# Performance work log

Measured on AMD Instinct MI355X. Metric: run time of the kernel, lower is better.

The kernel has to match this reference:

```python
import jax, jax.numpy as jnp
import numpy as np

N, T, H, L, E, F, CN, CG = 20000, 2, 128, 4, 320000, 514, 3, 2
EPS = 1e-7  # GENConv message epsilon


def _ln(x, g, b):
    mu = jnp.mean(x, axis=-1, keepdims=True)
    var = jnp.mean((x - mu) ** 2, axis=-1, keepdims=True)
    return (x - mu) / jnp.sqrt(var + 1e-5) * g + b


def _genconv(x, src, dst, e, W1, b1, g1, be1, W2, b2, t, n):
    # message: relu(x_j + edge_attr) + eps
    msg = jax.nn.relu(x[src] + e) + EPS  # [E,H]
    # softmax aggregation with learnable temperature t, grouped by dst
    logits = msg * t
    m = jax.ops.segment_max(logits, dst, num_segments=n)
    m = jnp.where(jnp.isfinite(m), m, 0.0)  # guard empty segments
    ex = jnp.exp(logits - m[dst])
    denom = jax.ops.segment_sum(ex, dst, num_segments=n)
    alpha = ex / (denom[dst] + 1e-16)
    agg = jax.ops.segment_sum(msg * alpha, dst, num_segments=n)  # [N,H]
    out = agg + x  # residual with root node (x_r)
    # MLP: Lin(H,2H) -> LayerNorm -> ReLU -> Lin(2H,H)
    h1 = jax.nn.relu(_ln(out @ W1 + b1, g1, be1))
    return h1 @ W2 + b2


def _attn(x, Wq, Wk, Wv, gamma):
    # x: [N, T, H]; channel (transform-axis) self-attention, gamma-gated residual
    q = jnp.einsum('tc,nch->nth', Wq, x)
    k = jnp.einsum('tc,nch->nth', Wk, x)
    v = jnp.einsum('tc,nch->nth', Wv, x)
    a = jax.nn.softmax(jnp.einsum('nth,nsh->nts', q, k), axis=-1)
    o = jnp.einsum('nts,nsh->nth', a, v)
    return gamma * o + x


def setup_inputs() -> dict:
    key = jax.random.key(0)
    ks = iter(jax.random.split(key, 48))

    def nrm(sh, s=0.02):
        return jax.random.normal(next(ks), sh, dtype=jnp.float32) * s

    inp = {}
    inp['node_feature'] = jax.random.normal(next(ks), (N, F), dtype=jnp.float32)
    inp['edge_index'] = jax.random.randint(next(ks), (T, 2, E), 0, N, dtype=jnp.int32)
    inp['edge_attr'] = jax.random.normal(next(ks), (T, E, 2), dtype=jnp.float32)
    # encoders
    inp['Wne'] = nrm((F, H)); inp['bne'] = jnp.zeros((H,), jnp.float32)
    inp['Wee'] = nrm((2, H)); inp['bee'] = jnp.zeros((H,), jnp.float32)
    # per-layer GENConv MLP params (stacked over L)
    inp['W1'] = nrm((L, H, 2 * H)); inp['b1'] = jnp.zeros((L, 2 * H), jnp.float32)
    inp['g1'] = jnp.ones((L, 2 * H), jnp.float32); inp['be1'] = jnp.zeros((L, 2 * H), jnp.float32)
    inp['W2'] = nrm((L, 2 * H, H)); inp['b2'] = jnp.zeros((L, H), jnp.float32)
    # DeepGCNLayer LayerNorms
    inp['dg'] = jnp.ones((L, H), jnp.float32); inp['db'] = jnp.zeros((L, H), jnp.float32)
    # learnable temperatures
    inp['t'] = jnp.ones((L,), jnp.float32)
    # node attention + head
    inp['Wq_n'] = nrm((T, T), 0.2); inp['Wk_n'] = nrm((T, T), 0.2); inp['Wv_n'] = nrm((T, T), 0.2)
    inp['gamma_n'] = jnp.float32(0.5)
    inp['Wn1'] = nrm((T * H, T * H)); inp['bn1'] = jnp.zeros((T * H,), jnp.float32)
    inp['Wn2'] = nrm((T * H, CN)); inp['bn2'] = jnp.zeros((CN,), jnp.float32)
    # graph attention + head
    inp['Wq_g'] = nrm((T, T), 0.2); inp['Wk_g'] = nrm((T, T), 0.2); inp['Wv_g'] = nrm((T, T), 0.2)
    inp['gamma_g'] = jnp.float32(0.5)
    inp['Wg1'] = nrm((T * H, T * H)); inp['bg1'] = jnp.zeros((T * H,), jnp.float32)
    inp['Wg2'] = nrm((T * H, CG)); inp['bg2'] = jnp.zeros((CG,), jnp.float32)
    return inp


def reference(node_feature, edge_index, edge_attr, Wne, bne, Wee, bee,
              W1, b1, g1, be1, W2, b2, dg, db, t,
              Wq_n, Wk_n, Wv_n, gamma_n, Wn1, bn1, Wn2, bn2,
              Wq_g, Wk_g, Wv_g, gamma_g, Wg1, bg1, Wg2, bg2):
    embs = []
    for ti in range(T):
        x = node_feature @ Wne + bne           # node_encoder
        e = edge_attr[ti] @ Wee + bee          # edge_encoder
        src, dst = edge_index[ti, 0], edge_index[ti, 1]
        # layers[0].conv applied directly
        x = _genconv(x, src, dst, e, W1[0], b1[0], g1[0], be1[0], W2[0], b2[0], t[0], N)
        # res+ DeepGCN blocks
        for l in range(1, L):
            h = jax.nn.relu(_ln(x, dg[l], db[l]))  # dropout p=0.1 is identity in eval
            x = x + _genconv(h, src, dst, e, W1[l], b1[l], g1[l], be1[l], W2[l], b2[l], t[l], N)
        x = jax.nn.relu(_ln(x, dg[0], db[0]))
        embs.append(x)
    emb = jnp.stack(embs, axis=1)  # [N, T, H]

    a = _attn(emb, Wq_n, Wk_n, Wv_n, gamma_n).reshape(N, T * H)
    node = jax.nn.relu(a @ Wn1 + bn1) @ Wn2 + bn2
    node = jax.nn.log_softmax(node, axis=-1)

    g = _attn(emb, Wq_g, Wk_g, Wv_g, gamma_g).reshape(N, T * H)
    gp = jnp.mean(g, axis=0, keepdims=True)  # global_mean_pool (single graph)
    gp = jax.nn.relu(gp @ Wg1 + bg1) @ Wg2 + bg2
    gp = jax.nn.log_softmax(gp, axis=-1)
    return (node, gp)
```

## Files before the change

kernel.cpp:

```cpp
#include <hip/hip_runtime.h>

#define NN 20000
#define TT 2
#define HH 128
#define LL 4
#define EE 320000
#define FF 514
#define CN 3
#define CG 2
#define EPS_MSG 1e-7f
#define MP 20096

typedef __bf16 bf16x8 __attribute__((ext_vector_type(8)));
typedef __bf16 bf16x4 __attribute__((ext_vector_type(4)));
typedef __bf16 bf16x2 __attribute__((ext_vector_type(2)));
typedef float f32x4 __attribute__((ext_vector_type(4)));

struct __align__(8) Edge { int src; __bf16 ea0, ea1; };

__device__ inline float wave_sum(float v) {
#pragma unroll
  for (int off = 32; off; off >>= 1) v += __shfl_xor(v, off);
  return v;
}
__device__ inline float red16(float v) {
  v += __shfl_xor(v, 1); v += __shfl_xor(v, 2);
  v += __shfl_xor(v, 4); v += __shfl_xor(v, 8);
  return v;
}

__device__ __forceinline__ float fexp2(float x) {
#if __has_builtin(__builtin_amdgcn_exp2f)
  return __builtin_amdgcn_exp2f(x);
#else
  return exp2f(x);
#endif
}

__device__ __forceinline__ void gload_lds16(const void* g, void* l) {
  __builtin_amdgcn_global_load_lds(
      (const __attribute__((address_space(1))) unsigned int*)g,
      (__attribute__((address_space(3))) unsigned int*)l, 16, 0, 0);
}

#define ENCB (MP / 64)
#define SCB 2500
#define CHUNK 5000
__global__ __launch_bounds__(256) void enc_scatter_kernel(
    const __bf16* __restrict__ A, const __bf16* __restrict__ BT,
    const float* __restrict__ bias, __bf16* __restrict__ C,
    const int* __restrict__ edge_index, const float* __restrict__ edge_attr,
    int* __restrict__ cursor, Edge* __restrict__ edges) {
  __shared__ __bf16 As[2][64][32];
  __shared__ __bf16 Bs[2][128][32];
  const int tid = threadIdx.x;
  if (blockIdx.x >= ENCB) {
    int chunk = blockIdx.x & 7;
    int i = ((blockIdx.x - ENCB) >> 3) * 256 + tid;
    if (i >= 2 * EE) return;
    int ti = (i >= EE) ? 1 : 0;
    int e = i - ti * EE;
    const int* srcp = edge_index + (size_t)ti * 2 * EE;
    int d = srcp[EE + e];
    int gnode = ti * NN + d;
    if (gnode / CHUNK != chunk) return;
    int s = srcp[e];
    float2 ea = ((const float2*)edge_attr)[(size_t)ti * EE + e];
    int pos = atomicAdd(&cursor[gnode], 1);
    Edge ed;
    ed.src = s + ti * MP;
    ed.ea0 = (__bf16)ea.x; ed.ea1 = (__bf16)ea.y;
    __builtin_memcpy(&edges[pos], &ed, sizeof(Edge));
    return;
  }
  const int K = 576;
  const int lane = tid & 63, w = tid >> 6;
  const int bm = blockIdx.x * 64;
  const int wr = (w >> 1) * 32, wc = (w & 1) * 64;
  const int fr = lane & 15, fq = lane >> 4;
  const int rowA = tid >> 2, chA = (tid & 3) * 8;
  const __bf16* Ab = A + (size_t)(bm + rowA) * K + chA;
  const __bf16* Bb = BT + (size_t)rowA * K + chA;
  const __bf16* Bb2 = Bb + (size_t)64 * K;
  f32x4 acc[2][4] = {};
#define STAGE(buf, k0)                                  \
  do {                                                  \
    gload_lds16(Ab + (k0), &As[buf][rowA][chA]);        \
    gload_lds16(Bb + (k0), &Bs[buf][rowA][chA]);        \
    gload_lds16(Bb2 + (k0), &Bs[buf][rowA + 64][chA]);  \
  } while (0)
  STAGE(0, 0);
  __syncthreads();
  int cur = 0;
  for (int k0 = 0; k0 < K; k0 += 32) {
    if (k0 + 32 < K) STAGE(cur ^ 1, k0 + 32);
    bf16x8 af[2], bq[4];
#pragma unroll
    for (int m = 0; m < 2; ++m)
      af[m] = *(const bf16x8*)&As[cur][wr + m * 16 + fr][fq * 8];
#pragma unroll
    for (int n = 0; n < 4; ++n)
      bq[n] = *(const bf16x8*)&Bs[cur][wc + n * 16 + fr][fq * 8];
#pragma unroll
    for (int m = 0; m < 2; ++m)
#pragma unroll
      for (int n = 0; n < 4; ++n)
        acc[m][n] =
            __builtin_amdgcn_mfma_f32_16x16x32_bf16(af[m], bq[n], acc[m][n], 0, 0, 0);
    __syncthreads();
    cur ^= 1;
  }
#undef STAGE
#pragma unroll
  for (int m = 0; m < 2; ++m) {
#pragma unroll
    for (int n = 0; n < 4; ++n) {
#pragma unroll
      for (int j = 0; j < 4; ++j) {
        int gm = bm + wr + m * 16 + fq * 4 + j;
        int gn = wc + n * 16 + fr;
        if (gm < NN) {
          __bf16 c = (__bf16)(acc[m][n][j] + bias[gn]);
          C[(size_t)gm * 128 + gn] = c;
          C[(size_t)(gm + MP) * 128 + gn] = c;
        }
      }
    }
  }
}

template <int EPI>
__global__ __launch_bounds__(256) void gemm256(
    const __bf16* __restrict__ A, const __bf16* __restrict__ BT,
    const float* __restrict__ bias, const float* __restrict__ g,
    const float* __restrict__ be, const float* __restrict__ W2h,
    const float* __restrict__ b2h, void* __restrict__ outp, int M, int K) {
  __shared__ __bf16 As[2][64][32];
  __shared__ __bf16 Bs[2][256][32];
  const int tid = threadIdx.x;
  const int lane = tid & 63, w = tid >> 6;
  const int bm = blockIdx.x * 64;
  const int wr = w * 16;
  const int fr = lane & 15, fq = lane >> 4;
  const int rowA = tid >> 2, chA = (tid & 3) * 8;
  const __bf16* Ab = A + (size_t)(bm + rowA) * K + chA;
  const __bf16* Bb = BT + (size_t)rowA * K + chA;
  f32x4 acc[16] = {};

#define STG(buf, k0)                                                \
  do {                                                              \
    gload_lds16(Ab + (k0), &As[buf][rowA][chA]);                    \
    _Pragma("unroll") for (int r = 0; r < 4; ++r)                   \
        gload_lds16(Bb + (size_t)(r * 64) * K + (k0),               \
                    &Bs[buf][rowA + r * 64][chA]);                  \
  } while (0)

  STG(0, 0);
  __syncthreads();
  int cur = 0;
  for (int k0 = 0; k0 < K; k0 += 32) {
    if (k0 + 32 < K) STG(cur ^ 1, k0 + 32);
    bf16x8 af = *(const bf16x8*)&As[cur][wr + fr][fq * 8];
#pragma unroll
    for (int n = 0; n < 16; ++n) {
      bf16x8 bq = *(const bf16x8*)&Bs[cur][n * 16 + fr][fq * 8];
      acc[n] = __builtin_amdgcn_mfma_f32_16x16x32_bf16(af, bq, acc[n], 0, 0, 0);
    }
    __syncthreads();
    cur ^= 1;
  }
#undef STG

  float cb[16];
#pragma unroll
  for (int n = 0; n < 16; ++n) cb[n] = bias[n * 16 + fr];

  if constexpr (EPI == 0) {
    float gv[16], bev[16];
#pragma unroll
    for (int n = 0; n < 16; ++n) {
      gv[n] = g[n * 16 + fr];
      bev[n] = be[n * 16 + fr];
    }
    __bf16* outb = (__bf16*)outp;
#pragma unroll
    for (int j = 0; j < 4; ++j) {
      float cj[16], s = 0.f, s2 = 0.f;
#pragma unroll
      for (int n = 0; n < 16; ++n) {
        float c = acc[n][j] + cb[n];
        cj[n] = c; s += c; s2 += c * c;
      }
      s = red16(s); s2 = red16(s2);
      float mu = s * (1.f / 256);
      float var = fmaxf(s2 * (1.f / 256) - mu * mu, 0.f);
      float rr = rsqrtf(var + 1e-5f);
      int gm = bm + wr + fq * 4 + j;
      __bf16* op = outb + (size_t)gm * 256;
#pragma unroll
      for (int n = 0; n < 16; ++n) {
        float y = (cj[n] - mu) * rr * gv[n] + bev[n];
        op[n * 16 + fr] = (__bf16)fmaxf(y, 0.f);
      }
    }
  } else {
    float w0[16], w1[16], w2[16];
#pragma unroll
    for (int n = 0; n < 16; ++n) {
      int col = n * 16 + fr;
      w0[n] = W2h[col * 3 + 0];
      w1[n] = W2h[col * 3 + 1];
      w2[n] = W2h[col * 3 + 2];
    }
    float* outf = (float*)outp;
#pragma unroll
    for (int j = 0; j < 4; ++j) {
      float p0 = 0.f, p1 = 0.f, p2 = 0.f;
#pragma unroll
      for (int n = 0; n < 16; ++n) {
        float h = fmaxf(acc[n][j] + cb[n], 0.f);
        p0 += h * w0[n]; p1 += h * w1[n]; p2 += h * w2[n];
      }
      p0 = red16(p0); p1 = red16(p1); p2 = red16(p2);
      int gm = bm + wr + fq * 4 + j;
      if (fr == 0 && gm < M) {
        float l0 = p0 + b2h[0], l1 = p1 + b2h[1], l2 = p2 + b2h[2];
        float m = fmaxf(l0, fmaxf(l1, l2));
        float lse = m + logf(__expf(l0 - m) + __expf(l1 - m) + __expf(l2 - m));
        outf[(size_t)gm * 3 + 0] = l0 - lse;
        outf[(size_t)gm * 3 + 1] = l1 - lse;
        outf[(size_t)gm * 3 + 2] = l2 - lse;
      }
    }
  }
}

template <int MODE>
__global__ __launch_bounds__(256) void gemm_lin2(
    const __bf16* __restrict__ A, const __bf16* __restrict__ BT,
    const float* __restrict__ bias, float* __restrict__ xres,
    const float* __restrict__ g, const float* __restrict__ be,
    void* __restrict__ lnout) {
  __shared__ __bf16 As[2][64][32];
  __shared__ __bf16 Bs[2][128][32];
  __shared__ float redS[64][2], redS2[64][2];
  const int tid = threadIdx.x;
  const int lane = tid & 63, w = tid >> 6;
  const int bm = blockIdx.x * 64;
  const int wr = (w >> 1) * 32, wc = (w & 1) * 64;
  const int fr = lane & 15, fq = lane >> 4;
  const int rowA = tid >> 2, chA = (tid & 3) * 8;
  const __bf16* Ab = A + (size_t)(bm + rowA) * 256 + chA;
  const __bf16* Bb = BT + (size_t)rowA * 256 + chA;
  const __bf16* Bb2 = Bb + (size_t)64 * 256;
  f32x4 acc[2][4] = {};

#define STAGE(buf, k0)                                  \
  do {                                                  \
    gload_lds16(Ab + (k0), &As[buf][rowA][chA]);        \
    gload_lds16(Bb + (k0), &Bs[buf][rowA][chA]);        \
    gload_lds16(Bb2 + (k0), &Bs[buf][rowA + 64][chA]);  \
  } while (0)

  STAGE(0, 0);
  __syncthreads();
  int cur = 0;
  for (int k0 = 0; k0 < 256; k0 += 32) {
    if (k0 + 32 < 256) STAGE(cur ^ 1, k0 + 32);
    bf16x8 af[2], bq[4];
#pragma unroll
    for (int m = 0; m < 2; ++m)
      af[m] = *(const bf16x8*)&As[cur][wr + m * 16 + fr][fq * 8];
#pragma unroll
    for (int n = 0; n < 4; ++n)
      bq[n] = *(const bf16x8*)&Bs[cur][wc + n * 16 + fr][fq * 8];
#pragma unroll
    for (int m = 0; m < 2; ++m)
#pragma unroll
      for (int n = 0; n < 4; ++n)
        acc[m][n] =
            __builtin_amdgcn_mfma_f32_16x16x32_bf16(af[m], bq[n], acc[m][n], 0, 0, 0);
    __syncthreads();
    cur ^= 1;
  }
#undef STAGE

  float cv[2][4][4];
#pragma unroll
  for (int m = 0; m < 2; ++m) {
    int r0 = wr + m * 16 + fq * 4;
#pragma unroll
    for (int j = 0; j < 4; ++j) {
      int gm = bm + r0 + j;
      float s = 0.f, s2 = 0.f;
#pragma unroll
      for (int n = 0; n < 4; ++n) {
        float c = acc[m][n][j] + bias[wc + n * 16 + fr];
        if (MODE != 0) c += xres[(size_t)gm * 128 + wc + n * 16 + fr];
        cv[m][n][j] = c;
        s += c; s2 += c * c;
      }
      s = red16(s); s2 = red16(s2);
      if (fr == 0) {
        redS[r0 + j][w & 1] = s;
        redS2[r0 + j][w & 1] = s2;
      }
    }
  }
  __syncthreads();
#pragma unroll
  for (int m = 0; m < 2; ++m) {
    int r0 = wr + m * 16 + fq * 4;
#pragma unroll
    for (int j = 0; j < 4; ++j) {
      int r = r0 + j;
      int gm = bm + r;
      float S = redS[r][0] + redS[r][1];
      float S2 = redS2[r][0] + redS2[r][1];
      float mu = S * (1.f / 128);
      float var = fmaxf(S2 * (1.f / 128) - mu * mu, 0.f);
      float rr = rsqrtf(var + 1e-5f);
      if constexpr (MODE < 2) {
        float* xp = xres + (size_t)gm * 128;
        __bf16* hp = (__bf16*)lnout + (size_t)gm * 128;
#pragma unroll
        for (int n = 0; n < 4; ++n) {
          int col = wc + n * 16 + fr;
          float c = cv[m][n][j];
          xp[col] = c;
          float y = (c - mu) * rr * g[col] + be[col];
          hp[col] = (__bf16)fmaxf(y, 0.f);
        }
      } else {
        int half = gm >= MP;
        int node = gm - half * MP;
        if (node < NN) {
          float* ep = (float*)lnout + (size_t)node * 256 + half * 128;
#pragma unroll
          for (int n = 0; n < 4; ++n) {
            int col = wc + n * 16 + fr;
            float y = (cv[m][n][j] - mu) * rr * g[col] + be[col];
            ep[col] = fmaxf(y, 0.f);
          }
        }
      }
    }
  }
}

struct WtDesc { const float* src; __bf16* dst; int K, N, Kpad; };
struct WtDescs { WtDesc d[10]; };
#define NF2B 20079
#define PADB 2422
#define WTB 2880
#define CNTB 2500

__global__ void prep_kernel(const float* __restrict__ nf_src,
                            __bf16* __restrict__ nf_dst, WtDescs descs,
                            const int* __restrict__ edge_index,
                            int* __restrict__ deg, float* __restrict__ gp_sum) {
  int b = blockIdx.x, tid = threadIdx.x;
  if (b < NF2B) {
    int i = b * 256 + tid;
    if (i >= NN * FF / 2) return;
    int row = i / 257;
    int col = (i - row * 257) * 2;
    float2 v = ((const float2*)nf_src)[i];
    bf16x2 o; o[0] = (__bf16)v.x; o[1] = (__bf16)v.y;
    *(bf16x2*)(nf_dst + (size_t)row * 576 + col) = o;
  } else if (b < NF2B + PADB) {
    int i = (b - NF2B) * 256 + tid;
    if (i >= NN * 31) return;
    int row = i / 31, j = i - row * 31;
    bf16x2 z; z[0] = (__bf16)0.f; z[1] = (__bf16)0.f;
    *(bf16x2*)(nf_dst + (size_t)row * 576 + 514 + 2 * j) = z;
  } else if (b < NF2B + PADB + WTB) {
    int wb = b - NF2B - PADB;
    WtDesc de = descs.d[wb / 288];
    int idx = (wb % 288) * 256 + tid;
    if (idx >= de.N * de.Kpad) return;
    int n = idx / de.Kpad, k = idx - n * de.Kpad;
    float v = (k < de.K) ? de.src[(size_t)k * de.N + n] : 0.f;
    de.dst[idx] = (__bf16)v;
  } else if (b < NF2B + PADB + WTB + CNTB) {
    int i = (b - NF2B - PADB - WTB) * 256 + tid;
    if (i >= 2 * EE) return;
    int ti = (i >= EE) ? 1 : 0;
    int e = i - ti * EE;
    int d = edge_index[(size_t)ti * 2 * EE + EE + e];
    atomicAdd(&deg[ti * NN + d], 1);
  } else {
    gp_sum[tid] = 0.f;
  }
}

__global__ __launch_bounds__(1024) void scan2_kernel(
    const int* __restrict__ deg_all, int* __restrict__ rowptr,
    int* __restrict__ cursor) {
  const int ti = blockIdx.x;
  const int* deg = deg_all + ti * NN;
  __shared__ int sums[1024];
  int tid = threadIdx.x;
  int chunk = (NN + 1023) / 1024;
  int begin = tid * chunk, end = min(begin + chunk, NN);
  int s = 0;
  for (int i = begin; i < end; ++i) s += deg[i];
  sums[tid] = s;
  __syncthreads();
  for (int off = 1; off < 1024; off <<= 1) {
    int v = (tid >= off) ? sums[tid - off] : 0;
    __syncthreads();
    sums[tid] += v;
    __syncthreads();
  }
  int running = ti * EE + sums[tid] - s;
  for (int i = begin; i < end; ++i) {
    rowptr[ti * NN + i] = running;
    cursor[ti * NN + i] = running;
    running += deg[i];
  }
  if (tid == 0 && ti == 1) rowptr[2 * NN] = 2 * EE;
}

__global__ __launch_bounds__(256) void agg_kernel(
    const __bf16* __restrict__ xin, const int* __restrict__ rowptr,
    const Edge* __restrict__ edges, const float* __restrict__ Wee,
    const float* __restrict__ bee, const float* __restrict__ tptr, int layer,
    __bf16* __restrict__ out) {
  int wave = threadIdx.x >> 6, lane = threadIdx.x & 63;
  int b = blockIdx.x;
  int x8 = b & 7;
  int q = x8 >> 1;
  int par = x8 & 1;
  int ti = q >> 1, chh = q & 1;
  int group = (b >> 3) * 2 + par;
  int node = group * 4 + wave;
  int gnode = ti * NN + node;
  int xrow = ti * MP + node;
  float t2 = tptr[layer] * 1.4426950408889634f;
  int qq = lane >> 4, c15 = lane & 15;
  int c0 = chh * 64 + c15 * 4;
  float w0[4], w1[4], bv[4];
#pragma unroll
  for (int i = 0; i < 4; ++i) {
    w0[i] = Wee[c0 + i];
    w1[i] = Wee[HH + c0 + i];
    bv[i] = bee[c0 + i];
  }
  float den[4] = {}, num[4] = {};
  int e = rowptr[gnode], e1 = rowptr[gnode + 1];

#define MLP4(XV, ED)                                                \
  do {                                                              \
    float eax = (float)(ED).ea0, eay = (float)(ED).ea1;             \
    _Pragma("unroll") for (int i = 0; i < 4; ++i) {                 \
      float m = (float)(XV)[i] + eax * w0[i] + eay * w1[i] + bv[i]; \
      m = fmaxf(m, 0.f) + EPS_MSG;                                  \
      float ex = fexp2(m * t2);                                     \
      den[i] += ex; num[i] += m * ex;                               \
    }                                                               \
  } while (0)

  for (; e + 8 <= e1; e += 8) {
    Edge E0 = edges[e + qq];
    Edge E1 = edges[e + 4 + qq];
    bf16x4 x0 = *(const bf16x4*)(xin + (size_t)E0.src * HH + c0);
    bf16x4 x1 = *(const bf16x4*)(xin + (size_t)E1.src * HH + c0);
    MLP4(x0, E0);
    MLP4(x1, E1);
  }
  if (e + qq < e1) {
    Edge E0 = edges[e + qq];
    bf16x4 x0 = *(const bf16x4*)(xin + (size_t)E0.src * HH + c0);
    MLP4(x0, E0);
  }
  if (e + 4 + qq < e1) {
    Edge E0 = edges[e + 4 + qq];
    bf16x4 x0 = *(const bf16x4*)(xin + (size_t)E0.src * HH + c0);
    MLP4(x0, E0);
  }
#undef MLP4

#pragma unroll
  for (int i = 0; i < 4; ++i) {
    den[i] += __shfl_xor(den[i], 16);
    den[i] += __shfl_xor(den[i], 32);
    num[i] += __shfl_xor(num[i], 16);
    num[i] += __shfl_xor(num[i], 32);
  }
  if (qq == 0) {
    bf16x4 xr = *(const bf16x4*)(xin + (size_t)xrow * HH + c0);
    bf16x4 o;
#pragma unroll
    for (int i = 0; i < 4; ++i)
      o[i] = (__bf16)(num[i] / (den[i] + 1e-16f) + (float)xr[i]);
    *(bf16x4*)(out + (size_t)xrow * HH + c0) = o;
  }
}

__global__ __launch_bounds__(256) void attn2_kernel(
    const float* __restrict__ emb, const float* __restrict__ Wq_n,
    const float* __restrict__ Wk_n, const float* __restrict__ Wv_n,
    const float* __restrict__ gn, const float* __restrict__ Wq_g,
    const float* __restrict__ Wk_g, const float* __restrict__ Wv_g,
    const float* __restrict__ gg, __bf16* __restrict__ outn,
    float* __restrict__ partial) {
  __shared__ float gsum[4][256];
  int wave = threadIdx.x >> 6, lane = threadIdx.x & 63;
  int tid = threadIdx.x;
  int n = blockIdx.x * 4 + wave;
  int c0 = lane * 2;
  const float* base = emb + (size_t)n * (2 * HH);
  float2 x0 = *(const float2*)(base + c0);
  float2 x1 = *(const float2*)(base + HH + c0);

#define ATTN_BODY(Wq, Wk, Wv, GAM, O0A, O0B, O1A, O1B)                        \
  {                                                                           \
    float gamma = *(GAM);                                                     \
    float wq00 = Wq[0], wq01 = Wq[1], wq10 = Wq[2], wq11 = Wq[3];             \
    float wk00 = Wk[0], wk01 = Wk[1], wk10 = Wk[2], wk11 = Wk[3];             \
    float wv00 = Wv[0], wv01 = Wv[1], wv10 = Wv[2], wv11 = Wv[3];             \
    float q0a = wq00 * x0.x + wq01 * x1.x, q0b = wq00 * x0.y + wq01 * x1.y;   \
    float q1a = wq10 * x0.x + wq11 * x1.x, q1b = wq10 * x0.y + wq11 * x1.y;   \
    float k0a = wk00 * x0.x + wk01 * x1.x, k0b = wk00 * x0.y + wk01 * x1.y;   \
    float k1a = wk10 * x0.x + wk11 * x1.x, k1b = wk10 * x0.y + wk11 * x1.y;   \
    float v0a = wv00 * x0.x + wv01 * x1.x, v0b = wv00 * x0.y + wv01 * x1.y;   \
    float v1a = wv10 * x0.x + wv11 * x1.x, v1b = wv10 * x0.y + wv11 * x1.y;   \
    float s00 = wave_sum(q0a * k0a + q0b * k0b);                              \
    float s01 = wave_sum(q0a * k1a + q0b * k1b);                              \
    float s10 = wave_sum(q1a * k0a + q1b * k0b);                              \
    float s11 = wave_sum(q1a * k1a + q1b * k1b);                              \
    float m0 = fmaxf(s00, s01);                                               \
    float e00 = __expf(s00 - m0), e01 = __expf(s01 - m0);                     \
    float i0 = 1.f / (e00 + e01);                                             \
    float a00 = e00 * i0, a01 = e01 * i0;                                     \
    float m1 = fmaxf(s10, s11);                                               \
    float e10 = __expf(s10 - m1), e11 = __expf(s11 - m1);                     \
    float i1 = 1.f / (e10 + e11);                                             \
    float a10 = e10 * i1, a11 = e11 * i1;                                     \
    O0A = gamma * (a00 * v0a + a01 * v1a) + x0.x;                             \
    O0B = gamma * (a00 * v0b + a01 * v1b) + x0.y;                             \
    O1A = gamma * (a10 * v0a + a11 * v1a) + x1.x;                             \
    O1B = gamma * (a10 * v0b + a11 * v1b) + x1.y;                             \
  }

  float n0a, n0b, n1a, n1b;
  ATTN_BODY(Wq_n, Wk_n, Wv_n, gn, n0a, n0b, n1a, n1b);
  __bf16* opn = outn + (size_t)n * (2 * HH);
  bf16x2 t0; t0[0] = (__bf16)n0a; t0[1] = (__bf16)n0b;
  bf16x2 t1; t1[0] = (__bf16)n1a; t1[1] = (__bf16)n1b;
  *(bf16x2*)(opn + c0) = t0;
  *(bf16x2*)(opn + HH + c0) = t1;

  float g0a, g0b, g1a, g1b;
  ATTN_BODY(Wq_g, Wk_g, Wv_g, gg, g0a, g0b, g1a, g1b);
  gsum[wave][c0] = g0a;
  gsum[wave][c0 + 1] = g0b;
  gsum[wave][128 + c0] = g1a;
  gsum[wave][129 + c0] = g1b;
  __syncthreads();
  partial[(size_t)blockIdx.x * 256 + tid] =
      gsum[0][tid] + gsum[1][tid] + gsum[2][tid] + gsum[3][tid];
#undef ATTN_BODY
}

__global__ __launch_bounds__(256) void pool_kernel(const float* __restrict__ partial,
                                                   float* __restrict__ gp_sum,
                                                   int nRows) {
  int c = threadIdx.x;
  float s = 0.f;
  for (int r = blockIdx.x; r < nRows; r += gridDim.x)
    s += partial[(size_t)r * 256 + c];
  atomicAdd(&gp_sum[c], s);
}

__global__ __launch_bounds__(256) void graph_head_kernel(
    const float* __restrict__ gp_sum, const float* __restrict__ Wg1,
    const float* __restrict__ bg1, const float* __restrict__ Wg2,
    const float* __restrict__ bg2, float* __restrict__ outp, float invN) {
  __shared__ float gp[256];
  __shared__ float h1[256];
  __shared__ float lg[2];
  int tid = threadIdx.x;
  gp[tid] = gp_sum[tid] * invN;
  __syncthreads();
  float acc = bg1[tid];
  for (int k = 0; k < 256; ++k) acc += gp[k] * Wg1[k * 256 + tid];
  h1[tid] = fmaxf(acc, 0.f);
  __syncthreads();
  if (tid < 2) {
    float l = bg2[tid];
    for (int c = 0; c < 256; ++c) l += h1[c] * Wg2[c * 2 + tid];
    lg[tid] = l;
  }
  __syncthreads();
  if (tid == 0) {
    float m = fmaxf(lg[0], lg[1]);
    float lse = m + logf(__expf(lg[0] - m) + __expf(lg[1] - m));
    outp[0] = lg[0] - lse;
    outp[1] = lg[1] - lse;
  }
}

extern "C" void kernel_launch(void* const* d_in, const int* in_sizes, int n_in,
                              void* d_out, int out_size, void* d_ws, size_t ws_size,
                              hipStream_t stream) {
  (void)in_sizes; (void)n_in; (void)out_size; (void)ws_size;
  const float* node_feature = (const float*)d_in[0];
  const int* edge_index = (const int*)d_in[1];
  const float* edge_attr = (const float*)d_in[2];
  const float* Wne = (const float*)d_in[3];
  const float* bne = (const float*)d_in[4];
  const float* Wee = (const float*)d_in[5];
  const float* bee = (const float*)d_in[6];
  const float* W1 = (const float*)d_in[7];
  const float* b1 = (const float*)d_in[8];
  const float* g1 = (const float*)d_in[9];
  const float* be1 = (const float*)d_in[10];
  const float* W2 = (const float*)d_in[11];
  const float* b2 = (const float*)d_in[12];
  const float* dg = (const float*)d_in[13];
  const float* db = (const float*)d_in[14];
  const float* tpar = (const float*)d_in[15];
  const float* Wq_n = (const float*)d_in[16];
  const float* Wk_n = (const float*)d_in[17];
  const float* Wv_n = (const float*)d_in[18];
  const float* gamma_n = (const float*)d_in[19];
  const float* Wn1 = (const float*)d_in[20];
  const float* bn1 = (const float*)d_in[21];
  const float* Wn2 = (const float*)d_in[22];
  const float* bn2 = (const float*)d_in[23];
  const float* Wq_g = (const float*)d_in[24];
  const float* Wk_g = (const float*)d_in[25];
  const float* Wv_g = (const float*)d_in[26];
  const float* gamma_g = (const float*)d_in[27];
  const float* Wg1 = (const float*)d_in[28];
  const float* bg1 = (const float*)d_in[29];
  const float* Wg2 = (const float*)d_in[30];
  const float* bg2 = (const float*)d_in[31];
  float* out = (float*)d_out;

  char* pc = (char*)d_ws;
  auto alloc = [&](size_t bytes) {
    char* r = pc;
    pc += (bytes + 255) & ~(size_t)255;
    return r;
  };
  float* xbuf = (float*)alloc((size_t)2 * MP * HH * 4);
  __bf16* hbuf_b = (__bf16*)alloc((size_t)2 * MP * HH * 2);
  __bf16* t256_b = (__bf16*)alloc((size_t)2 * MP * 256 * 2);
  float* emb = (float*)alloc((size_t)NN * 2 * HH * 4);
  __bf16* aggout_b = (__bf16*)alloc((size_t)2 * MP * HH * 2);
  __bf16* nf_b = (__bf16*)emb;
  __bf16* attnb = t256_b;
  float* partial = xbuf;
  __bf16* wt_ne = (__bf16*)alloc((size_t)128 * 576 * 2);
  __bf16* wt1 = (__bf16*)alloc((size_t)4 * 256 * 128 * 2);
  __bf16* wt2 = (__bf16*)alloc((size_t)4 * 128 * 256 * 2);
  __bf16* wtn1 = (__bf16*)alloc((size_t)256 * 256 * 2);
  float* gp_sum = (float*)alloc(256 * 4);
  int* deg = (int*)alloc((size_t)2 * NN * 4);
  int* cursor = (int*)alloc((size_t)2 * NN * 4);
  int* rowptr = (int*)alloc((size_t)(2 * NN + 2) * 4);
  Edge* edges = (Edge*)alloc((size_t)2 * EE * 8);

  const int gRows2 = 2 * MP / 64;

  WtDescs wd;
  wd.d[0] = {Wne, wt_ne, FF, HH, 576};
  for (int l = 0; l < 4; ++l)
    wd.d[1 + l] = {W1 + (size_t)l * HH * 256, wt1 + (size_t)l * 256 * HH, HH, 256, HH};
  for (int l = 0; l < 4; ++l)
    wd.d[5 + l] = {W2 + (size_t)l * 256 * HH, wt2 + (size_t)l * HH * 256, 256, HH, 256};
  wd.d[9] = {Wn1, wtn1, 256, 256, 256};

  hipMemsetAsync(deg, 0, 2 * NN * sizeof(int), stream);
  prep_kernel<<<NF2B + PADB + WTB + CNTB + 1, 256, 0, stream>>>(
      node_feature, nf_b, wd, edge_index, deg, gp_sum);
  scan2_kernel<<<2, 1024, 0, stream>>>(deg, rowptr, cursor);
  enc_scatter_kernel<<<ENCB + 8 * SCB, 256, 0, stream>>>(
      nf_b, wt_ne, bne, hbuf_b, edge_index, edge_attr, cursor, edges);

  for (int l = 0; l < LL; ++l) {
    agg_kernel<<<2500 * 8, 256, 0, stream>>>(hbuf_b, rowptr, edges, Wee, bee, tpar,
                                             l, aggout_b);
    gemm256<0><<<gRows2, 256, 0, stream>>>(aggout_b, wt1 + (size_t)l * 256 * HH,
                                           b1 + l * 2 * HH, g1 + l * 2 * HH,
                                           be1 + l * 2 * HH, nullptr, nullptr, t256_b,
                                           2 * MP, HH);
    const __bf16* w2l = wt2 + (size_t)l * HH * 256;
    const float* b2l = b2 + l * HH;
    if (l == 0)
      gemm_lin2<0><<<gRows2, 256, 0, stream>>>(t256_b, w2l, b2l, xbuf, dg + 1 * HH,
                                               db + 1 * HH, hbuf_b);
    else if (l < LL - 1)
      gemm_lin2<1><<<gRows2, 256, 0, stream>>>(t256_b, w2l, b2l, xbuf,
                                               dg + (l + 1) * HH, db + (l + 1) * HH,
                                               hbuf_b);
    else
      gemm_lin2<2><<<gRows2, 256, 0, stream>>>(t256_b, w2l, b2l, xbuf, dg, db, emb);
  }

  attn2_kernel<<<NN / 4, 256, 0, stream>>>(emb, Wq_n, Wk_n, Wv_n, gamma_n, Wq_g,
                                           Wk_g, Wv_g, gamma_g, attnb, partial);
  gemm256<1><<<MP / 64, 256, 0, stream>>>(attnb, wtn1, bn1, nullptr, nullptr, Wn2,
                                          bn2, out, NN, 256);
  pool_kernel<<<128, 256, 0, stream>>>(partial, gp_sum, NN / 4);
  graph_head_kernel<<<1, 256, 0, stream>>>(gp_sum, Wg1, bg1, Wg2, bg2,
                                           out + (size_t)NN * CN, 1.0f / NN);
}
```

Before: 487.9 us.

## Switch node features and edge records to fp32 and rework aggregation lane mapping

The hidden-state buffer read by the aggregation kernel and the CSR edge records now hold fp32 values instead of bf16 (edges grow from 8 to 16 bytes). The aggregation kernel is remapped so each wave covers 32 channels with 8 edge slots, and the edge-encoder weights are prescaled by the temperature so the exp argument comes from fused FMAs, with a fallback path when the temperature is not positive. This likely targets accuracy against the fp32 reference more than speed. It doubles gather and edge-record bandwidth in the memory-bound aggregation loop and drops the message epsilon in the positive-temperature path.

Result: slower. 596.6 us (+22.3%).

```diff
diff --git a/kernel.cpp b/kernel.cpp
--- a/kernel.cpp
+++ b/kernel.cpp
@@ -8,7 +8,6 @@
 #define FF 514
 #define CN 3
 #define CG 2
-#define EPS_MSG 1e-7f
 #define MP 20096
 
 typedef __bf16 bf16x8 __attribute__((ext_vector_type(8)));
@@ -16,7 +15,7 @@
 typedef __bf16 bf16x2 __attribute__((ext_vector_type(2)));
 typedef float f32x4 __attribute__((ext_vector_type(4)));
 
-struct __align__(8) Edge { int src; __bf16 ea0, ea1; };
+struct __align__(16) Edge16 { int src; float ea0, ea1; int pad; };
 
 __device__ inline float wave_sum(float v) {
 #pragma unroll
@@ -48,9 +47,9 @@
 #define CHUNK 5000
 __global__ __launch_bounds__(256) void enc_scatter_kernel(
     const __bf16* __restrict__ A, const __bf16* __restrict__ BT,
-    const float* __restrict__ bias, __bf16* __restrict__ C,
+    const float* __restrict__ bias, float* __restrict__ C,
     const int* __restrict__ edge_index, const float* __restrict__ edge_attr,
-    int* __restrict__ cursor, Edge* __restrict__ edges) {
+    int* __restrict__ cursor, Edge16* __restrict__ edges) {
   __shared__ __bf16 As[2][64][32];
   __shared__ __bf16 Bs[2][128][32];
   const int tid = threadIdx.x;
@@ -67,10 +66,10 @@
     int s = srcp[e];
     float2 ea = ((const float2*)edge_attr)[(size_t)ti * EE + e];
     int pos = atomicAdd(&cursor[gnode], 1);
-    Edge ed;
+    Edge16 ed;
     ed.src = s + ti * MP;
-    ed.ea0 = (__bf16)ea.x; ed.ea1 = (__bf16)ea.y;
-    __builtin_memcpy(&edges[pos], &ed, sizeof(Edge));
+    ed.ea0 = ea.x; ed.ea1 = ea.y; ed.pad = 0;
+    __builtin_memcpy(&edges[pos], &ed, sizeof(Edge16));
     return;
   }
   const int K = 576;
@@ -120,7 +119,7 @@
         int gm = bm + wr + m * 16 + fq * 4 + j;
         int gn = wc + n * 16 + fr;
         if (gm < NN) {
-          __bf16 c = (__bf16)(acc[m][n][j] + bias[gn]);
+          float c = acc[m][n][j] + bias[gn];
           C[(size_t)gm * 128 + gn] = c;
           C[(size_t)(gm + MP) * 128 + gn] = c;
         }
@@ -240,7 +239,7 @@
     const __bf16* __restrict__ A, const __bf16* __restrict__ BT,
     const float* __restrict__ bias, float* __restrict__ xres,
     const float* __restrict__ g, const float* __restrict__ be,
-    void* __restrict__ lnout) {
+    float* __restrict__ lnout) {
   __shared__ __bf16 As[2][64][32];
   __shared__ __bf16 Bs[2][128][32];
   __shared__ float redS[64][2], redS2[64][2];
@@ -322,20 +321,20 @@
       float rr = rsqrtf(var + 1e-5f);
       if constexpr (MODE < 2) {
         float* xp = xres + (size_t)gm * 128;
-        __bf16* hp = (__bf16*)lnout + (size_t)gm * 128;
+        float* hp = lnout + (size_t)gm * 128;
 #pragma unroll
         for (int n = 0; n < 4; ++n) {
           int col = wc + n * 16 + fr;
           float c = cv[m][n][j];
           xp[col] = c;
           float y = (c - mu) * rr * g[col] + be[col];
-          hp[col] = (__bf16)fmaxf(y, 0.f);
+          hp[col] = fmaxf(y, 0.f);
         }
       } else {
         int half = gm >= MP;
         int node = gm - half * MP;
         if (node < NN) {
-          float* ep = (float*)lnout + (size_t)node * 256 + half * 128;
+          float* ep = lnout + (size_t)node * 256 + half * 128;
 #pragma unroll
           for (int n = 0; n < 4; ++n) {
             int col = wc + n * 16 + fr;
@@ -423,78 +422,104 @@
 }
 
 __global__ __launch_bounds__(256) void agg_kernel(
-    const __bf16* __restrict__ xin, const int* __restrict__ rowptr,
-    const Edge* __restrict__ edges, const float* __restrict__ Wee,
+    const float* __restrict__ xin, const int* __restrict__ rowptr,
+    const Edge16* __restrict__ edges, const float* __restrict__ Wee,
     const float* __restrict__ bee, const float* __restrict__ tptr, int layer,
     __bf16* __restrict__ out) {
   int wave = threadIdx.x >> 6, lane = threadIdx.x & 63;
   int b = blockIdx.x;
-  int x8 = b & 7;
-  int q = x8 >> 1;
-  int par = x8 & 1;
-  int ti = q >> 1, chh = q & 1;
-  int group = (b >> 3) * 2 + par;
-  int node = group * 4 + wave;
+  int g8 = b & 7;
+  int ti = g8 >> 2, cq = g8 & 3;
+  int node = (b >> 3) * 4 + wave;
   int gnode = ti * NN + node;
   int xrow = ti * MP + node;
-  float t2 = tptr[layer] * 1.4426950408889634f;
-  int qq = lane >> 4, c15 = lane & 15;
-  int c0 = chh * 64 + c15 * 4;
-  float w0[4], w1[4], bv[4];
-#pragma unroll
-  for (int i = 0; i < 4; ++i) {
-    w0[i] = Wee[c0 + i];
-    w1[i] = Wee[HH + c0 + i];
-    bv[i] = bee[c0 + i];
-  }
+  float t = tptr[layer];
+  float t2 = t * 1.4426950408889634f;
+  int slot = lane >> 3, cl = lane & 7;
+  int c0 = cq * 32 + cl * 4;
   float den[4] = {}, num[4] = {};
-  int e = rowptr[gnode], e1 = rowptr[gnode + 1];
-
-#define MLP4(XV, ED)                                                \
-  do {                                                              \
-    float eax = (float)(ED).ea0, eay = (float)(ED).ea1;             \
-    _Pragma("unroll") for (int i = 0; i < 4; ++i) {                 \
-      float m = (float)(XV)[i] + eax * w0[i] + eay * w1[i] + bv[i]; \
-      m = fmaxf(m, 0.f) + EPS_MSG;                                  \
-      float ex = fexp2(m * t2);                                     \
-      den[i] += ex; num[i] += m * ex;                               \
-    }                                                               \
+  int e = rowptr[gnode];
+  const int e1 = rowptr[gnode + 1];
+
+  if (t2 > 0.f) {
+    float w0p[4], w1p[4], bvp[4];
+#pragma unroll
+    for (int i = 0; i < 4; ++i) {
+      w0p[i] = Wee[c0 + i] * t2;
+      w1p[i] = Wee[HH + c0 + i] * t2;
+      bvp[i] = bee[c0 + i] * t2;
+    }
+#define MLPF(E)                                                         \
+  do {                                                                  \
+    f32x4 xv = *(const f32x4*)(xin + (size_t)(E).src * HH + c0);        \
+    _Pragma("unroll") for (int i = 0; i < 4; ++i) {                     \
+      float te = fmaf((E).ea0, w0p[i], fmaf((E).ea1, w1p[i], bvp[i]));  \
+      float sm = fmaxf(fmaf(xv[i], t2, te), 0.f);                       \
+      float ex = fexp2(sm);                                             \
+      den[i] += ex; num[i] += sm * ex;                                  \
+    }                                                                   \
   } while (0)
-
-  for (; e + 8 <= e1; e += 8) {
-    Edge E0 = edges[e + qq];
-    Edge E1 = edges[e + 4 + qq];
-    bf16x4 x0 = *(const bf16x4*)(xin + (size_t)E0.src * HH + c0);
-    bf16x4 x1 = *(const bf16x4*)(xin + (size_t)E1.src * HH + c0);
-    MLP4(x0, E0);
-    MLP4(x1, E1);
-  }
-  if (e + qq < e1) {
-    Edge E0 = edges[e + qq];
-    bf16x4 x0 = *(const bf16x4*)(xin + (size_t)E0.src * HH + c0);
-    MLP4(x0, E0);
-  }
-  if (e + 4 + qq < e1) {
-    Edge E0 = edges[e + 4 + qq];
-    bf16x4 x0 = *(const bf16x4*)(xin + (size_t)E0.src * HH + c0);
-    MLP4(x0, E0);
-  }
-#undef MLP4
-
-#pragma unroll
-  for (int i = 0; i < 4; ++i) {
-    den[i] += __shfl_xor(den[i], 16);
-    den[i] += __shfl_xor(den[i], 32);
-    num[i] += __shfl_xor(num[i], 16);
-    num[i] += __shfl_xor(num[i], 32);
-  }
-  if (qq == 0) {
-    bf16x4 xr = *(const bf16x4*)(xin + (size_t)xrow * HH + c0);
-    bf16x4 o;
-#pragma unroll
-    for (int i = 0; i < 4; ++i)
-      o[i] = (__bf16)(num[i] / (den[i] + 1e-16f) + (float)xr[i]);
-    *(bf16x4*)(out + (size_t)xrow * HH + c0) = o;
+    for (; e + 8 <= e1; e += 8) {
+      Edge16 E = edges[e + slot];
+      MLPF(E);
+    }
+    if (e + slot < e1) {
+      Edge16 E = edges[e + slot];
+      MLPF(E);
+    }
+#undef MLPF
+#pragma unroll
+    for (int i = 0; i < 4; ++i) {
+      den[i] += __shfl_xor(den[i], 8);
+      den[i] += __shfl_xor(den[i], 16);
+      den[i] += __shfl_xor(den[i], 32);
+      num[i] += __shfl_xor(num[i], 8);
+      num[i] += __shfl_xor(num[i], 16);
+      num[i] += __shfl_xor(num[i], 32);
+    }
+    if (slot == 0) {
+      f32x4 xr = *(const f32x4*)(xin + (size_t)xrow * HH + c0);
+      bf16x4 o;
+#pragma unroll
+      for (int i = 0; i < 4; ++i)
+        o[i] = (__bf16)(num[i] / (t2 * (den[i] + 1e-16f)) + xr[i]);
+      *(bf16x4*)(out + (size_t)xrow * HH + c0) = o;
+    }
+  } else {
+    float w0[4], w1[4], bv[4];
+#pragma unroll
+    for (int i = 0; i < 4; ++i) {
+      w0[i] = Wee[c0 + i];
+      w1[i] = Wee[HH + c0 + i];
+      bv[i] = bee[c0 + i];
+    }
+    for (; e + slot < e1; e += 8) {
+      Edge16 E = edges[e + slot];
+      f32x4 xv = *(const f32x4*)(xin + (size_t)E.src * HH + c0);
+#pragma unroll
+      for (int i = 0; i < 4; ++i) {
+        float m = fmaxf(xv[i] + E.ea0 * w0[i] + E.ea1 * w1[i] + bv[i], 0.f) + 1e-7f;
+        float ex = fexp2(m * t2);
+        den[i] += ex; num[i] += m * ex;
+      }
+    }
+#pragma unroll
+    for (int i = 0; i < 4; ++i) {
+      den[i] += __shfl_xor(den[i], 8);
+      den[i] += __shfl_xor(den[i], 16);
+      den[i] += __shfl_xor(den[i], 32);
+      num[i] += __shfl_xor(num[i], 8);
+      num[i] += __shfl_xor(num[i], 16);
+      num[i] += __shfl_xor(num[i], 32);
+    }
+    if (slot == 0) {
+      f32x4 xr = *(const f32x4*)(xin + (size_t)xrow * HH + c0);
+      bf16x4 o;
+#pragma unroll
+      for (int i = 0; i < 4; ++i)
+        o[i] = (__bf16)(num[i] / (den[i] + 1e-16f) + xr[i]);
+      *(bf16x4*)(out + (size_t)xrow * HH + c0) = o;
+    }
   }
 }
 
@@ -647,7 +672,7 @@
     return r;
   };
   float* xbuf = (float*)alloc((size_t)2 * MP * HH * 4);
-  __bf16* hbuf_b = (__bf16*)alloc((size_t)2 * MP * HH * 2);
+  float* hbuf = (float*)alloc((size_t)2 * MP * HH * 4);
   __bf16* t256_b = (__bf16*)alloc((size_t)2 * MP * 256 * 2);
   float* emb = (float*)alloc((size_t)NN * 2 * HH * 4);
   __bf16* aggout_b = (__bf16*)alloc((size_t)2 * MP * HH * 2);
@@ -662,7 +687,7 @@
   int* deg = (int*)alloc((size_t)2 * NN * 4);
   int* cursor = (int*)alloc((size_t)2 * NN * 4);
   int* rowptr = (int*)alloc((size_t)(2 * NN + 2) * 4);
-  Edge* edges = (Edge*)alloc((size_t)2 * EE * 8);
+  Edge16* edges = (Edge16*)alloc((size_t)2 * EE * 16);
 
   const int gRows2 = 2 * MP / 64;
 
@@ -679,11 +704,11 @@
       node_feature, nf_b, wd, edge_index, deg, gp_sum);
   scan2_kernel<<<2, 1024, 0, stream>>>(deg, rowptr, cursor);
   enc_scatter_kernel<<<ENCB + 8 * SCB, 256, 0, stream>>>(
-      nf_b, wt_ne, bne, hbuf_b, edge_index, edge_attr, cursor, edges);
+      nf_b, wt_ne, bne, hbuf, edge_index, edge_attr, cursor, edges);
 
   for (int l = 0; l < LL; ++l) {
-    agg_kernel<<<2500 * 8, 256, 0, stream>>>(hbuf_b, rowptr, edges, Wee, bee, tpar,
-                                             l, aggout_b);
+    agg_kernel<<<8 * (NN / 4), 256, 0, stream>>>(hbuf, rowptr, edges, Wee, bee,
+                                                 tpar, l, aggout_b);
     gemm256<0><<<gRows2, 256, 0, stream>>>(aggout_b, wt1 + (size_t)l * 256 * HH,
                                            b1 + l * 2 * HH, g1 + l * 2 * HH,
                                            be1 + l * 2 * HH, nullptr, nullptr, t256_b,
@@ -692,11 +717,11 @@
     const float* b2l = b2 + l * HH;
     if (l == 0)
       gemm_lin2<0><<<gRows2, 256, 0, stream>>>(t256_b, w2l, b2l, xbuf, dg + 1 * HH,
-                                               db + 1 * HH, hbuf_b);
+                                               db + 1 * HH, hbuf);
     else if (l < LL - 1)
       gemm_lin2<1><<<gRows2, 256, 0, stream>>>(t256_b, w2l, b2l, xbuf,
                                                dg + (l + 1) * HH, db + (l + 1) * HH,
-                                               hbuf_b);
+                                               hbuf);
     else
       gemm_lin2<2><<<gRows2, 256, 0, stream>>>(t256_b, w2l, b2l, xbuf, dg, db, emb);
   }
```
